# Performance work log

Hardware: AMD Instinct MI355X
Metric: run time of the kernel (lower is better)

## Reference

```python
import jax, jax.numpy as jnp
import numpy as np

IN_DIM = 1024
HEAD_DIM = 64
NUM_HEADS = 16
SEQ = 4096


def setup_inputs() -> dict:
    key = jax.random.key(0)
    ks = jax.random.split(key, 7)
    s = 1.0 / np.sqrt(IN_DIM)
    return {
        "h": jax.random.normal(ks[0], (SEQ, IN_DIM), dtype=jnp.float32),
        "Wq": jax.random.uniform(ks[1], (IN_DIM, NUM_HEADS * HEAD_DIM), jnp.float32, -s, s),
        "Wk": jax.random.uniform(ks[2], (IN_DIM, NUM_HEADS * HEAD_DIM), jnp.float32, -s, s),
        "Wv": jax.random.uniform(ks[3], (IN_DIM, NUM_HEADS * HEAD_DIM), jnp.float32, -s, s),
        "bq": jax.random.uniform(ks[4], (NUM_HEADS * HEAD_DIM,), jnp.float32, -s, s),
        "bk": jax.random.uniform(ks[5], (NUM_HEADS * HEAD_DIM,), jnp.float32, -s, s),
        "bv": jax.random.uniform(ks[6], (NUM_HEADS * HEAD_DIM,), jnp.float32, -s, s),
    }


def reference(h, Wq, Wk, Wv, bq, bk, bv):
    n = h.shape[0]
    # QKV projections -> [H, S, D]
    q = (h @ Wq + bq).reshape(n, NUM_HEADS, HEAD_DIM).transpose(1, 0, 2)
    k = (h @ Wk + bk).reshape(n, NUM_HEADS, HEAD_DIM).transpose(1, 0, 2)
    v = (h @ Wv + bv).reshape(n, NUM_HEADS, HEAD_DIM).transpose(1, 0, 2)
    scale = 1.0 / np.sqrt(HEAD_DIM).astype(np.float32)
    scores = jnp.einsum('hsd,htd->hst', q, k) * scale  # [H, S, S]
    probs = jax.nn.softmax(scores, axis=-1)
    out = jnp.einsum('hst,htd->hsd', probs, v)  # [H, S, D]
    return out.transpose(1, 0, 2).reshape(n, NUM_HEADS * HEAD_DIM)
```

## Files before the change

kernel.cpp:

```cpp
#include <hip/hip_runtime.h>
#include <hip/hip_bf16.h>

#define IN_DIM    1024
#define HEAD_DIM  64
#define NUM_HEADS 16
#define SEQ       4096

#define QSCALE 0.18033688011112042f

typedef __bf16 bf16;
typedef __attribute__((ext_vector_type(4))) __bf16 bf16x4;
typedef __attribute__((ext_vector_type(8))) __bf16 bf16x8;
typedef __attribute__((ext_vector_type(4))) float floatx4;
typedef __attribute__((ext_vector_type(16))) float floatx16;
typedef __attribute__((ext_vector_type(4))) unsigned uint32x4;

__device__ __forceinline__ void async16(bf16* lds, const bf16* g) {
    __builtin_amdgcn_global_load_lds(
        (const __attribute__((address_space(1))) unsigned int*)g,
        (__attribute__((address_space(3))) unsigned int*)lds, 16, 0, 0);
}

__device__ __forceinline__ unsigned cvtpk_bf16(float lo, float hi) {
    unsigned r;
    asm("v_cvt_pk_bf16_f32 %0, %1, %2" : "=v"(r) : "v"(lo), "v"(hi));
    return r;
}

__device__ __forceinline__ void permswap(unsigned& a, unsigned& b) {
    asm("v_permlane32_swap_b32 %0, %1" : "+v"(a), "+v"(b));
}


__global__ void mha_conv_h(const float* __restrict__ h, bf16* __restrict__ hb) {
    int i = blockIdx.x * blockDim.x + threadIdx.x;
    float4 v = ((const float4*)h)[i];
    bf16x4 r;
    r[0] = (bf16)v.x; r[1] = (bf16)v.y; r[2] = (bf16)v.z; r[3] = (bf16)v.w;
    ((bf16x4*)hb)[i] = r;
}

__global__ void mha_conv_wt(const float* __restrict__ Wq, const float* __restrict__ Wk,
                            const float* __restrict__ Wv, bf16* __restrict__ Wt) {
    __shared__ bf16 tile[64][65];
    const int mat = blockIdx.z;
    const float* W = (mat == 0) ? Wq : (mat == 1) ? Wk : Wv;
    const int k0 = blockIdx.y * 64, n0 = blockIdx.x * 64;
    const int tn = threadIdx.x & 63, tq = threadIdx.x >> 6;
#pragma unroll
    for (int i = 0; i < 16; ++i) {
        int kk = tq + i * 4;
        tile[kk][tn] = (bf16)W[(size_t)(k0 + kk) * 1024 + n0 + tn];
    }
    __syncthreads();
#pragma unroll
    for (int i = 0; i < 16; ++i) {
        int nn = tq + i * 4;
        Wt[((size_t)mat << 20) + (size_t)(n0 + nn) * 1024 + k0 + tn] = tile[tn][nn];
    }
}

__launch_bounds__(256)
__global__ void mha_qkv_gemm(const bf16* __restrict__ hb, const bf16* __restrict__ Wt,
                             const float* __restrict__ bq, const float* __restrict__ bk,
                             const float* __restrict__ bv,
                             bf16* __restrict__ Qb, bf16* __restrict__ Kb,
                             bf16* __restrict__ Vt) {
    __shared__ __align__(16) bf16 As[128 * 32];
    __shared__ __align__(16) bf16 Bs[128 * 32];

    const int lane = threadIdx.x & 63;
    const int wave = threadIdx.x >> 6;
    const int l16  = lane & 15;
    const int quad = lane >> 4;
    const int wm   = wave & 1;
    const int wn   = wave >> 1;

    const int m0  = blockIdx.x * 128;
    const int n0  = blockIdx.y * 128;
    const int mat = n0 >> 10;
    const int nc0 = n0 & 1023;

    const bf16* Wp = Wt + ((size_t)mat << 20);

    floatx4 acc[4][4] = {};
    const int swz = (l16 >> 1) & 3;

    for (int k0 = 0; k0 < IN_DIM; k0 += 32) {
#pragma unroll
        for (int r = 0; r < 2; ++r) {
            int g = wave * 128 + r * 64 + lane;
            int row = g >> 2, c = g & 3;
            int gc = c ^ ((row >> 1) & 3);
            bf16* ldsbase_a = As + (size_t)(wave * 128 + r * 64) * 8;
            bf16* ldsbase_b = Bs + (size_t)(wave * 128 + r * 64) * 8;
            async16(ldsbase_a, hb + (size_t)(m0 + row) * IN_DIM + k0 + gc * 8);
            async16(ldsbase_b, Wp + (size_t)(nc0 + row) * IN_DIM + k0 + gc * 8);
        }
        __syncthreads();

        bf16x8 af[4], bf[4];
#pragma unroll
        for (int mt = 0; mt < 4; ++mt)
            af[mt] = *(const bf16x8*)(As + (size_t)(wm * 64 + mt * 16 + l16) * 32
                                      + ((quad ^ swz) * 8));
#pragma unroll
        for (int nt = 0; nt < 4; ++nt)
            bf[nt] = *(const bf16x8*)(Bs + (size_t)(wn * 64 + nt * 16 + l16) * 32
                                      + ((quad ^ swz) * 8));
#pragma unroll
        for (int mt = 0; mt < 4; ++mt)
#pragma unroll
            for (int nt = 0; nt < 4; ++nt)
                acc[mt][nt] = __builtin_amdgcn_mfma_f32_16x16x32_bf16(af[mt], bf[nt],
                                                                      acc[mt][nt], 0, 0, 0);
        __syncthreads();
    }

    const float* bias = (mat == 0) ? bq : (mat == 1) ? bk : bv;
#pragma unroll
    for (int nt = 0; nt < 4; ++nt) {
        int nc = nc0 + wn * 64 + nt * 16 + l16;
        float bb = bias[nc];
        int head = nc >> 6, d = nc & 63;
#pragma unroll
        for (int mt = 0; mt < 4; ++mt)
#pragma unroll
            for (int r = 0; r < 4; ++r) {
                int srow = m0 + wm * 64 + mt * 16 + quad * 4 + r;
                float v = acc[mt][nt][r] + bb;
                if (mat == 0)
                    Qb[((size_t)head * SEQ + srow) * HEAD_DIM + d] = (bf16)(v * QSCALE);
                else if (mat == 1)
                    Kb[((size_t)head * SEQ + srow) * HEAD_DIM + d] = (bf16)v;
                else
                    Vt[((size_t)head * HEAD_DIM + d) * SEQ + srow] = (bf16)v;
            }
    }
}

__launch_bounds__(512)
__global__ void mha_attn(const bf16* __restrict__ Qb, const bf16* __restrict__ Kb,
                         const bf16* __restrict__ Vt, float* __restrict__ out) {
    __shared__ __align__(16) bf16 Ks[3][64 * 64];
    __shared__ __align__(16) bf16 Vs[3][64 * 64];

    const int lane = threadIdx.x & 63;
    const int wave = threadIdx.x >> 6;
    const int l31  = lane & 31;
    const int hi   = lane >> 5;

    const int bid = blockIdx.x;
    const int hh  = 2 * (bid & 7) + ((bid >> 3) & 1);
    const int qx  = bid >> 4;
    const int q0  = qx * 256 + wave * 32;

    const bf16* Qh = Qb + (size_t)hh * SEQ * HEAD_DIM;
    const bf16* Kh = Kb + (size_t)hh * SEQ * HEAD_DIM;
    const bf16* Vh = Vt + (size_t)hh * HEAD_DIM * SEQ;

    const int sg   = wave * 64 + lane;
    const int srow = sg >> 3;
    const int sgc  = (sg & 7) ^ (srow & 7);

    bf16x8 qf[4];
#pragma unroll
    for (int ks = 0; ks < 4; ++ks)
        qf[ks] = *(const bf16x8*)(Qh + (size_t)(q0 + l31) * HEAD_DIM + ks * 16 + hi * 8);

    bf16x8 vone;
#pragma unroll
    for (int i = 0; i < 8; ++i) vone[i] = (bf16)1.0f;

    floatx16 o0 = {}, o1 = {}, ol = {};
    const int swz = l31 & 7;

    async16(&Ks[0][wave * 512], Kh + (size_t)srow * HEAD_DIM + sgc * 8);
    async16(&Vs[0][wave * 512], Vh + (size_t)srow * SEQ + 0 + sgc * 8);
    async16(&Ks[1][wave * 512], Kh + (size_t)(64 + srow) * HEAD_DIM + sgc * 8);
    async16(&Vs[1][wave * 512], Vh + (size_t)srow * SEQ + 64 + sgc * 8);
    asm volatile("s_waitcnt vmcnt(0)" ::: "memory");
    __builtin_amdgcn_s_barrier();

    int cur = 0;
    for (int t = 0; t < SEQ / 64; ++t) {
        int pre = cur + 2; if (pre >= 3) pre -= 3;
        if (t + 2 < SEQ / 64) {
            const int tg = (t + 2) * 64;
            async16(&Ks[pre][wave * 512], Kh + (size_t)(tg + srow) * HEAD_DIM + sgc * 8);
            async16(&Vs[pre][wave * 512], Vh + (size_t)srow * SEQ + tg + sgc * 8);
        }
        if (t < SEQ / 64 - 2)      asm volatile("s_waitcnt vmcnt(4)" ::: "memory");
        else if (t == SEQ / 64 - 2) asm volatile("s_waitcnt vmcnt(2)" ::: "memory");
        else                        asm volatile("s_waitcnt vmcnt(0)" ::: "memory");
        __builtin_amdgcn_s_barrier();
        asm volatile("" ::: "memory");

        bf16x8 kf[2][4];
#pragma unroll
        for (int tt = 0; tt < 2; ++tt)
#pragma unroll
            for (int ks = 0; ks < 4; ++ks)
                kf[tt][ks] = *(const bf16x8*)(&Ks[cur][(tt * 32 + l31) * 64
                                              + (((ks * 2 + hi) ^ swz) * 8)]);

        floatx16 s0 = {}, s1 = {};
#pragma unroll
        for (int ks = 0; ks < 4; ++ks)
            s0 = __builtin_amdgcn_mfma_f32_32x32x16_bf16(kf[0][ks], qf[ks], s0, 0, 0, 0);
#pragma unroll
        for (int ks = 0; ks < 4; ++ks)
            s1 = __builtin_amdgcn_mfma_f32_32x32x16_bf16(kf[1][ks], qf[ks], s1, 0, 0, 0);

        bf16x8 vf[2][4];
#pragma unroll
        for (int dt = 0; dt < 2; ++dt)
#pragma unroll
            for (int sl = 0; sl < 4; ++sl)
                vf[dt][sl] = *(const bf16x8*)(&Vs[cur][(dt * 32 + l31) * 64
                                              + (((sl * 2 + hi) ^ swz) * 8)]);

        bf16x8 pa[4];
#pragma unroll
        for (int sl = 0; sl < 4; ++sl) {
            const floatx16 sv = (sl < 2) ? s0 : s1;
            const int rb = 8 * (sl & 1);
            float p0 = __builtin_amdgcn_exp2f(sv[rb + 0]);
            float p1 = __builtin_amdgcn_exp2f(sv[rb + 1]);
            float p2 = __builtin_amdgcn_exp2f(sv[rb + 2]);
            float p3 = __builtin_amdgcn_exp2f(sv[rb + 3]);
            float p4 = __builtin_amdgcn_exp2f(sv[rb + 4]);
            float p5 = __builtin_amdgcn_exp2f(sv[rb + 5]);
            float p6 = __builtin_amdgcn_exp2f(sv[rb + 6]);
            float p7 = __builtin_amdgcn_exp2f(sv[rb + 7]);
            unsigned u0 = cvtpk_bf16(p0, p1);
            unsigned u1 = cvtpk_bf16(p2, p3);
            unsigned u2 = cvtpk_bf16(p4, p5);
            unsigned u3 = cvtpk_bf16(p6, p7);
            permswap(u0, u2);
            permswap(u1, u3);
            uint32x4 w;
            w[0] = u0; w[1] = u1; w[2] = u2; w[3] = u3;
            pa[sl] = __builtin_bit_cast(bf16x8, w);
        }

#pragma unroll
        for (int sl = 0; sl < 4; ++sl) {
            o0 = __builtin_amdgcn_mfma_f32_32x32x16_bf16(pa[sl], vf[0][sl], o0, 0, 0, 0);
            o1 = __builtin_amdgcn_mfma_f32_32x32x16_bf16(pa[sl], vf[1][sl], o1, 0, 0, 0);
            ol = __builtin_amdgcn_mfma_f32_32x32x16_bf16(pa[sl], vone, ol, 0, 0, 0);
        }

        asm volatile("" ::: "memory");
        __builtin_amdgcn_s_barrier();
        cur = cur + 1; if (cur == 3) cur = 0;
    }

#pragma unroll
    for (int r = 0; r < 16; ++r) {
        const int q = q0 + (r & 3) + 8 * (r >> 2) + 4 * hi;
        const float inv = 1.0f / ol[r];
        out[(size_t)q * (NUM_HEADS * HEAD_DIM) + hh * 64 + l31]      = o0[r] * inv;
        out[(size_t)q * (NUM_HEADS * HEAD_DIM) + hh * 64 + 32 + l31] = o1[r] * inv;
    }
}

extern "C" void kernel_launch(void* const* d_in, const int* in_sizes, int n_in,
                              void* d_out, int out_size, void* d_ws, size_t ws_size,
                              hipStream_t stream) {
    const float* h  = (const float*)d_in[0];
    const float* Wq = (const float*)d_in[1];
    const float* Wk = (const float*)d_in[2];
    const float* Wv = (const float*)d_in[3];
    const float* bq = (const float*)d_in[4];
    const float* bk = (const float*)d_in[5];
    const float* bv = (const float*)d_in[6];
    float* out = (float*)d_out;

    char* ws = (char*)d_ws;
    const size_t MB = 1024 * 1024;
    bf16* hb = (bf16*)(ws);
    bf16* Wt = (bf16*)(ws + 8 * MB);
    bf16* Qb = (bf16*)(ws + 14 * MB);
    bf16* Kb = (bf16*)(ws + 22 * MB);
    bf16* Vt = (bf16*)(ws + 30 * MB);

    mha_conv_h<<<(SEQ * IN_DIM / 4) / 256, 256, 0, stream>>>(h, hb);
    mha_conv_wt<<<dim3(16, 16, 3), 256, 0, stream>>>(Wq, Wk, Wv, Wt);
    mha_qkv_gemm<<<dim3(SEQ / 128, (3 * IN_DIM) / 128), 256, 0, stream>>>(
        hb, Wt, bq, bk, bv, Qb, Kb, Vt);
    mha_attn<<<dim3((SEQ / 256) * NUM_HEADS), 512, 0, stream>>>(Qb, Kb, Vt, out);
}
```

Baseline: 206.5 us.

## Split attention KV range across two blocks and merge with atomics

Each attention block now processes only half of the key/value sequence, doubling the grid to 512 blocks so each CU can host more waves. Partial unnormalized outputs and denominators are combined with float atomicAdd into zeroed workspace buffers, and a separate kernel normalizes into the output. This trades better occupancy and latency hiding for extra zeroing, atomic traffic, and a normalization pass over the full output.

```diff
diff --git a/kernel.cpp b/kernel.cpp
--- a/kernel.cpp
+++ b/kernel.cpp
@@ -31,6 +31,13 @@
     asm("v_permlane32_swap_b32 %0, %1" : "+v"(a), "+v"(b));
 }
 
+
+__global__ void mha_zero(float4* __restrict__ p, int n4) {
+    const float4 z = {0.f, 0.f, 0.f, 0.f};
+    for (int i = blockIdx.x * blockDim.x + threadIdx.x; i < n4;
+         i += gridDim.x * blockDim.x)
+        p[i] = z;
+}
 
 __global__ void mha_conv_h(const float* __restrict__ h, bf16* __restrict__ hb) {
     int i = blockIdx.x * blockDim.x + threadIdx.x;
@@ -139,9 +146,12 @@
     }
 }
 
+#define NT (SEQ / 64 / 2)
+
 __launch_bounds__(512)
 __global__ void mha_attn(const bf16* __restrict__ Qb, const bf16* __restrict__ Kb,
-                         const bf16* __restrict__ Vt, float* __restrict__ out) {
+                         const bf16* __restrict__ Vt, float* __restrict__ num,
+                         float* __restrict__ denom) {
     __shared__ __align__(16) bf16 Ks[3][64 * 64];
     __shared__ __align__(16) bf16 Vs[3][64 * 64];
 
@@ -150,10 +160,14 @@
     const int l31  = lane & 31;
     const int hi   = lane >> 5;
 
-    const int bid = blockIdx.x;
-    const int hh  = 2 * (bid & 7) + ((bid >> 3) & 1);
-    const int qx  = bid >> 4;
-    const int q0  = qx * 256 + wave * 32;
+    const int bid  = blockIdx.x;
+    const int xcd  = bid & 7;
+    const int inner = bid >> 3;
+    const int hh   = 2 * xcd + (inner & 1);
+    const int half = (inner >> 1) & 1;
+    const int qx   = inner >> 2;
+    const int q0   = qx * 256 + wave * 32;
+    const int tb   = half * (SEQ / 2);
 
     const bf16* Qh = Qb + (size_t)hh * SEQ * HEAD_DIM;
     const bf16* Kh = Kb + (size_t)hh * SEQ * HEAD_DIM;
@@ -175,24 +189,24 @@
     floatx16 o0 = {}, o1 = {}, ol = {};
     const int swz = l31 & 7;
 
-    async16(&Ks[0][wave * 512], Kh + (size_t)srow * HEAD_DIM + sgc * 8);
-    async16(&Vs[0][wave * 512], Vh + (size_t)srow * SEQ + 0 + sgc * 8);
-    async16(&Ks[1][wave * 512], Kh + (size_t)(64 + srow) * HEAD_DIM + sgc * 8);
-    async16(&Vs[1][wave * 512], Vh + (size_t)srow * SEQ + 64 + sgc * 8);
+    async16(&Ks[0][wave * 512], Kh + (size_t)(tb + srow) * HEAD_DIM + sgc * 8);
+    async16(&Vs[0][wave * 512], Vh + (size_t)srow * SEQ + tb + sgc * 8);
+    async16(&Ks[1][wave * 512], Kh + (size_t)(tb + 64 + srow) * HEAD_DIM + sgc * 8);
+    async16(&Vs[1][wave * 512], Vh + (size_t)srow * SEQ + tb + 64 + sgc * 8);
     asm volatile("s_waitcnt vmcnt(0)" ::: "memory");
     __builtin_amdgcn_s_barrier();
 
     int cur = 0;
-    for (int t = 0; t < SEQ / 64; ++t) {
+    for (int t = 0; t < NT; ++t) {
         int pre = cur + 2; if (pre >= 3) pre -= 3;
-        if (t + 2 < SEQ / 64) {
-            const int tg = (t + 2) * 64;
+        if (t + 2 < NT) {
+            const int tg = tb + (t + 2) * 64;
             async16(&Ks[pre][wave * 512], Kh + (size_t)(tg + srow) * HEAD_DIM + sgc * 8);
             async16(&Vs[pre][wave * 512], Vh + (size_t)srow * SEQ + tg + sgc * 8);
         }
-        if (t < SEQ / 64 - 2)      asm volatile("s_waitcnt vmcnt(4)" ::: "memory");
-        else if (t == SEQ / 64 - 2) asm volatile("s_waitcnt vmcnt(2)" ::: "memory");
-        else                        asm volatile("s_waitcnt vmcnt(0)" ::: "memory");
+        if (t < NT - 2)       asm volatile("s_waitcnt vmcnt(4)" ::: "memory");
+        else if (t == NT - 2) asm volatile("s_waitcnt vmcnt(2)" ::: "memory");
+        else                  asm volatile("s_waitcnt vmcnt(0)" ::: "memory");
         __builtin_amdgcn_s_barrier();
         asm volatile("" ::: "memory");
 
@@ -259,10 +273,23 @@
 #pragma unroll
     for (int r = 0; r < 16; ++r) {
         const int q = q0 + (r & 3) + 8 * (r >> 2) + 4 * hi;
-        const float inv = 1.0f / ol[r];
-        out[(size_t)q * (NUM_HEADS * HEAD_DIM) + hh * 64 + l31]      = o0[r] * inv;
-        out[(size_t)q * (NUM_HEADS * HEAD_DIM) + hh * 64 + 32 + l31] = o1[r] * inv;
-    }
+        float* np = num + (size_t)q * (NUM_HEADS * HEAD_DIM) + hh * 64;
+        atomicAdd(np + l31,      o0[r]);
+        atomicAdd(np + 32 + l31, o1[r]);
+        if (l31 == 0) atomicAdd(&denom[hh * SEQ + q], ol[r]);
+    }
+}
+
+__global__ void mha_norm(const float* __restrict__ num, const float* __restrict__ denom,
+                         float* __restrict__ out) {
+    const int i = blockIdx.x * blockDim.x + threadIdx.x;
+    const int flat = i * 4;
+    const int q = flat >> 10;
+    const int head = (flat & 1023) >> 6;
+    float4 n = ((const float4*)num)[i];
+    const float inv = 1.0f / denom[head * SEQ + q];
+    n.x *= inv; n.y *= inv; n.z *= inv; n.w *= inv;
+    ((float4*)out)[i] = n;
 }
 
 extern "C" void kernel_launch(void* const* d_in, const int* in_sizes, int n_in,
@@ -279,15 +306,20 @@
 
     char* ws = (char*)d_ws;
     const size_t MB = 1024 * 1024;
-    bf16* hb = (bf16*)(ws);
-    bf16* Wt = (bf16*)(ws + 8 * MB);
-    bf16* Qb = (bf16*)(ws + 14 * MB);
-    bf16* Kb = (bf16*)(ws + 22 * MB);
-    bf16* Vt = (bf16*)(ws + 30 * MB);
-
+    bf16*  hb    = (bf16*)(ws);
+    bf16*  Wt    = (bf16*)(ws + 8 * MB);
+    bf16*  Qb    = (bf16*)(ws + 14 * MB);
+    bf16*  Kb    = (bf16*)(ws + 22 * MB);
+    bf16*  Vt    = (bf16*)(ws + 30 * MB);
+    float* num   = (float*)(ws + 38 * MB);
+    float* denom = (float*)(ws + 54 * MB);
+
+    const int n4 = (16 * 1024 * 1024 + NUM_HEADS * SEQ * 4) / 16;
+    mha_zero<<<2048, 256, 0, stream>>>((float4*)num, n4);
     mha_conv_h<<<(SEQ * IN_DIM / 4) / 256, 256, 0, stream>>>(h, hb);
     mha_conv_wt<<<dim3(16, 16, 3), 256, 0, stream>>>(Wq, Wk, Wv, Wt);
     mha_qkv_gemm<<<dim3(SEQ / 128, (3 * IN_DIM) / 128), 256, 0, stream>>>(
         hb, Wt, bq, bk, bv, Qb, Kb, Vt);
-    mha_attn<<<dim3((SEQ / 256) * NUM_HEADS), 512, 0, stream>>>(Qb, Kb, Vt, out);
-}
+    mha_attn<<<dim3(512), 512, 0, stream>>>(Qb, Kb, Vt, num, denom);
+    mha_norm<<<(SEQ * NUM_HEADS * HEAD_DIM / 4) / 256, 256, 0, stream>>>(num, denom, out);
+}
```

Measured after the change: 226.7 us. 9.8% more time.

## Rewrite QKV GEMM with 256x256 tiles, double-buffered LDS and interleaved prefetch

Applied to the files above, without the earlier changes.

The QKV projection GEMM moves from 128x128 tiles with K-step 32 and two barriers per step to 256x256 tiles with K-step 64 over 512 threads. LDS is double-buffered, and global-to-LDS copies of the next K slice are spread across four MFMA phases, with s_setprio raised around the MFMA bursts. The aim is more data reuse per tile and overlap of memory latency with compute. In exchange the grid shrinks to 192 blocks (fewer than the CU count) and register pressure rises with 32 accumulators per wave.

```diff
diff --git a/kernel.cpp b/kernel.cpp
--- a/kernel.cpp
+++ b/kernel.cpp
@@ -60,74 +60,111 @@
     }
 }
 
-__launch_bounds__(256)
+#define GPHASE(KS, MH, READBF)                                                 \
+    {                                                                          \
+        bf16x8 af[4];                                                          \
+        _Pragma("unroll")                                                      \
+        for (int mtl = 0; mtl < 4; ++mtl)                                      \
+            af[mtl] = *(const bf16x8*)(&Abuf[cb][                              \
+                (wm * 128 + ((MH) * 4 + mtl) * 16 + l16) * 64                  \
+                + ((((KS) * 4 + quad) ^ swz) * 8)]);                           \
+        if (READBF) {                                                          \
+            _Pragma("unroll")                                                  \
+            for (int nt = 0; nt < 4; ++nt)                                     \
+                bfr[nt] = *(const bf16x8*)(&Bbuf[cb][                          \
+                    (wn * 64 + nt * 16 + l16) * 64                             \
+                    + ((((KS) * 4 + quad) ^ swz) * 8)]);                       \
+        }                                                                      \
+        __builtin_amdgcn_s_setprio(1);                                         \
+        _Pragma("unroll")                                                      \
+        for (int mtl = 0; mtl < 4; ++mtl)                                      \
+            _Pragma("unroll")                                                  \
+            for (int nt = 0; nt < 4; ++nt)                                     \
+                acc[(MH) * 4 + mtl][nt] =                                      \
+                    __builtin_amdgcn_mfma_f32_16x16x32_bf16(                   \
+                        af[mtl], bfr[nt], acc[(MH) * 4 + mtl][nt], 0, 0, 0);   \
+        __builtin_amdgcn_s_setprio(0);                                         \
+        asm volatile("" ::: "memory");                                         \
+        __builtin_amdgcn_s_barrier();                                          \
+    }
+
+__launch_bounds__(512)
 __global__ void mha_qkv_gemm(const bf16* __restrict__ hb, const bf16* __restrict__ Wt,
                              const float* __restrict__ bq, const float* __restrict__ bk,
                              const float* __restrict__ bv,
                              bf16* __restrict__ Qb, bf16* __restrict__ Kb,
                              bf16* __restrict__ Vt) {
-    __shared__ __align__(16) bf16 As[128 * 32];
-    __shared__ __align__(16) bf16 Bs[128 * 32];
-
-    const int lane = threadIdx.x & 63;
-    const int wave = threadIdx.x >> 6;
+    __shared__ __align__(16) bf16 Abuf[2][256 * 64];
+    __shared__ __align__(16) bf16 Bbuf[2][256 * 64];
+
+    const int tid  = threadIdx.x;
+    const int lane = tid & 63;
+    const int wave = tid >> 6;
     const int l16  = lane & 15;
-    const int quad = lane >> 4;
-    const int wm   = wave & 1;
-    const int wn   = wave >> 1;
-
-    const int m0  = blockIdx.x * 128;
-    const int n0  = blockIdx.y * 128;
-    const int mat = n0 >> 10;
-    const int nc0 = n0 & 1023;
-
-    const bf16* Wp = Wt + ((size_t)mat << 20);
-
-    floatx4 acc[4][4] = {};
-    const int swz = (l16 >> 1) & 3;
-
-    for (int k0 = 0; k0 < IN_DIM; k0 += 32) {
-#pragma unroll
-        for (int r = 0; r < 2; ++r) {
-            int g = wave * 128 + r * 64 + lane;
-            int row = g >> 2, c = g & 3;
-            int gc = c ^ ((row >> 1) & 3);
-            bf16* ldsbase_a = As + (size_t)(wave * 128 + r * 64) * 8;
-            bf16* ldsbase_b = Bs + (size_t)(wave * 128 + r * 64) * 8;
-            async16(ldsbase_a, hb + (size_t)(m0 + row) * IN_DIM + k0 + gc * 8);
-            async16(ldsbase_b, Wp + (size_t)(nc0 + row) * IN_DIM + k0 + gc * 8);
+    const int quad = (lane >> 4) & 3;
+    const int wm   = wave >> 2;
+    const int wn   = wave & 3;
+
+    const int m0  = blockIdx.x * 256;
+    const int by  = blockIdx.y;
+    const int mat = by >> 2;
+    const int nc0 = (by & 3) * 256;
+
+    const bf16* hb_blk = hb + (size_t)m0 * 1024;
+    const bf16* Wb_blk = Wt + ((size_t)mat << 20) + (size_t)nc0 * 1024;
+
+    const int crow = tid >> 3;
+    const int cs   = (tid & 7) ^ (crow & 7);
+    const int swz  = l16 & 7;
+
+    auto stage_half = [&](bf16* ldsb, const bf16* g) {
+        async16(ldsb + wave * 512,        g + (size_t)crow * 1024 + cs * 8);
+        async16(ldsb + 4096 + wave * 512, g + (size_t)(crow + 64) * 1024 + cs * 8);
+    };
+
+    floatx4 acc[8][4] = {};
+
+    stage_half(&Abuf[0][0],    hb_blk);
+    stage_half(&Abuf[0][8192], hb_blk + 128 * 1024);
+    stage_half(&Bbuf[0][0],    Wb_blk);
+    stage_half(&Bbuf[0][8192], Wb_blk + 128 * 1024);
+
+    for (int u = 0; u < 16; ++u) {
+        const int cb = u & 1, nb = cb ^ 1;
+        const size_t kn = (size_t)(u + 1) * 64;
+        bf16x8 bfr[4];
+
+        if (u < 15) {
+            stage_half(&Abuf[nb][0], hb_blk + kn);
+            asm volatile("s_waitcnt vmcnt(2)" ::: "memory");
+        } else {
+            asm volatile("s_waitcnt vmcnt(0)" ::: "memory");
         }
-        __syncthreads();
-
-        bf16x8 af[4], bf[4];
-#pragma unroll
-        for (int mt = 0; mt < 4; ++mt)
-            af[mt] = *(const bf16x8*)(As + (size_t)(wm * 64 + mt * 16 + l16) * 32
-                                      + ((quad ^ swz) * 8));
-#pragma unroll
-        for (int nt = 0; nt < 4; ++nt)
-            bf[nt] = *(const bf16x8*)(Bs + (size_t)(wn * 64 + nt * 16 + l16) * 32
-                                      + ((quad ^ swz) * 8));
-#pragma unroll
-        for (int mt = 0; mt < 4; ++mt)
-#pragma unroll
-            for (int nt = 0; nt < 4; ++nt)
-                acc[mt][nt] = __builtin_amdgcn_mfma_f32_16x16x32_bf16(af[mt], bf[nt],
-                                                                      acc[mt][nt], 0, 0, 0);
-        __syncthreads();
+        __builtin_amdgcn_s_barrier();
+        asm volatile("" ::: "memory");
+        GPHASE(0, 0, 1)
+
+        if (u < 15) stage_half(&Abuf[nb][8192], hb_blk + 128 * 1024 + kn);
+        GPHASE(0, 1, 0)
+
+        if (u < 15) stage_half(&Bbuf[nb][0], Wb_blk + kn);
+        GPHASE(1, 0, 1)
+
+        if (u < 15) stage_half(&Bbuf[nb][8192], Wb_blk + 128 * 1024 + kn);
+        GPHASE(1, 1, 0)
     }
 
     const float* bias = (mat == 0) ? bq : (mat == 1) ? bk : bv;
+    const int head = (nc0 >> 6) + wn;
 #pragma unroll
     for (int nt = 0; nt < 4; ++nt) {
-        int nc = nc0 + wn * 64 + nt * 16 + l16;
-        float bb = bias[nc];
-        int head = nc >> 6, d = nc & 63;
-#pragma unroll
-        for (int mt = 0; mt < 4; ++mt)
+        const int d  = nt * 16 + l16;
+        const float bb = bias[nc0 + wn * 64 + d];
+#pragma unroll
+        for (int mt = 0; mt < 8; ++mt)
 #pragma unroll
             for (int r = 0; r < 4; ++r) {
-                int srow = m0 + wm * 64 + mt * 16 + quad * 4 + r;
+                const int srow = m0 + wm * 128 + mt * 16 + quad * 4 + r;
                 float v = acc[mt][nt][r] + bb;
                 if (mat == 0)
                     Qb[((size_t)head * SEQ + srow) * HEAD_DIM + d] = (bf16)(v * QSCALE);
@@ -190,7 +227,7 @@
             async16(&Ks[pre][wave * 512], Kh + (size_t)(tg + srow) * HEAD_DIM + sgc * 8);
             async16(&Vs[pre][wave * 512], Vh + (size_t)srow * SEQ + tg + sgc * 8);
         }
-        if (t < SEQ / 64 - 2)      asm volatile("s_waitcnt vmcnt(4)" ::: "memory");
+        if (t < SEQ / 64 - 2)       asm volatile("s_waitcnt vmcnt(4)" ::: "memory");
         else if (t == SEQ / 64 - 2) asm volatile("s_waitcnt vmcnt(2)" ::: "memory");
         else                        asm volatile("s_waitcnt vmcnt(0)" ::: "memory");
         __builtin_amdgcn_s_barrier();
@@ -287,7 +324,7 @@
 
     mha_conv_h<<<(SEQ * IN_DIM / 4) / 256, 256, 0, stream>>>(h, hb);
     mha_conv_wt<<<dim3(16, 16, 3), 256, 0, stream>>>(Wq, Wk, Wv, Wt);
-    mha_qkv_gemm<<<dim3(SEQ / 128, (3 * IN_DIM) / 128), 256, 0, stream>>>(
+    mha_qkv_gemm<<<dim3(16, 12), 512, 0, stream>>>(
         hb, Wt, bq, bk, bv, Qb, Kb, Vt);
     mha_attn<<<dim3((SEQ / 256) * NUM_HEADS), 512, 0, stream>>>(Qb, Kb, Vt, out);
 }
```

Result: slower. 242.2 us (+17.3%).

## Give each attention wave 64 query rows, halving waves per block

Applied to the files above, without the earlier changes.

The attention kernel now runs 4 waves of 256 threads instead of 8, and each wave processes two 32-row query tiles that share the same K/V fragments read from LDS. This halves LDS reads of K and V per query row and doubles the cooperative load work per thread. It also makes the cvt and permlane inline asm volatile with explicit s_nop padding, which pins instruction ordering. In exchange it raises register pressure (launch bounds 256,1) and leaves fewer waves per CU to hide latency.

```diff
diff --git a/kernel.cpp b/kernel.cpp
--- a/kernel.cpp
+++ b/kernel.cpp
@@ -23,13 +23,38 @@
 
 __device__ __forceinline__ unsigned cvtpk_bf16(float lo, float hi) {
     unsigned r;
-    asm("v_cvt_pk_bf16_f32 %0, %1, %2" : "=v"(r) : "v"(lo), "v"(hi));
+    asm volatile("s_nop 1\n\tv_cvt_pk_bf16_f32 %0, %1, %2"
+                 : "=v"(r) : "v"(lo), "v"(hi));
     return r;
 }
 
 __device__ __forceinline__ void permswap(unsigned& a, unsigned& b) {
-    asm("v_permlane32_swap_b32 %0, %1" : "+v"(a), "+v"(b));
-}
+    asm volatile("s_nop 3\n\tv_permlane32_swap_b32 %0, %1" : "+v"(a), "+v"(b));
+}
+
+#define PACK(PA, S0, S1)                                                       \
+    _Pragma("unroll")                                                          \
+    for (int sl = 0; sl < 4; ++sl) {                                           \
+        const floatx16 sv = (sl < 2) ? (S0) : (S1);                            \
+        const int rb = 8 * (sl & 1);                                           \
+        float p0 = __builtin_amdgcn_exp2f(sv[rb + 0]);                         \
+        float p1 = __builtin_amdgcn_exp2f(sv[rb + 1]);                         \
+        float p2 = __builtin_amdgcn_exp2f(sv[rb + 2]);                         \
+        float p3 = __builtin_amdgcn_exp2f(sv[rb + 3]);                         \
+        float p4 = __builtin_amdgcn_exp2f(sv[rb + 4]);                         \
+        float p5 = __builtin_amdgcn_exp2f(sv[rb + 5]);                         \
+        float p6 = __builtin_amdgcn_exp2f(sv[rb + 6]);                         \
+        float p7 = __builtin_amdgcn_exp2f(sv[rb + 7]);                         \
+        unsigned u0 = cvtpk_bf16(p0, p1);                                      \
+        unsigned u1 = cvtpk_bf16(p2, p3);                                      \
+        unsigned u2 = cvtpk_bf16(p4, p5);                                      \
+        unsigned u3 = cvtpk_bf16(p6, p7);                                      \
+        permswap(u0, u2);                                                      \
+        permswap(u1, u3);                                                      \
+        uint32x4 w;                                                            \
+        w[0] = u0; w[1] = u1; w[2] = u2; w[3] = u3;                            \
+        (PA)[sl] = __builtin_bit_cast(bf16x8, w);                              \
+    }
 
 
 __global__ void mha_conv_h(const float* __restrict__ h, bf16* __restrict__ hb) {
@@ -139,7 +164,7 @@
     }
 }
 
-__launch_bounds__(512)
+__launch_bounds__(256, 1)
 __global__ void mha_attn(const bf16* __restrict__ Qb, const bf16* __restrict__ Kb,
                          const bf16* __restrict__ Vt, float* __restrict__ out) {
     __shared__ __align__(16) bf16 Ks[3][64 * 64];
@@ -153,32 +178,44 @@
     const int bid = blockIdx.x;
     const int hh  = 2 * (bid & 7) + ((bid >> 3) & 1);
     const int qx  = bid >> 4;
-    const int q0  = qx * 256 + wave * 32;
+    const int q0  = qx * 256 + wave * 64;
 
     const bf16* Qh = Qb + (size_t)hh * SEQ * HEAD_DIM;
     const bf16* Kh = Kb + (size_t)hh * SEQ * HEAD_DIM;
     const bf16* Vh = Vt + (size_t)hh * HEAD_DIM * SEQ;
 
-    const int sg   = wave * 64 + lane;
-    const int srow = sg >> 3;
-    const int sgc  = (sg & 7) ^ (srow & 7);
-
-    bf16x8 qf[4];
-#pragma unroll
-    for (int ks = 0; ks < 4; ++ks)
-        qf[ks] = *(const bf16x8*)(Qh + (size_t)(q0 + l31) * HEAD_DIM + ks * 16 + hi * 8);
+    const int ci0 = wave * 64 + lane;
+    const int r0c = ci0 >> 3;
+    const int sc0 = (ci0 & 7) ^ (r0c & 7);
+    const int r1c = r0c + 32;
+    const int sc1 = sc0;
+
+    bf16x8 qfa[4], qfb[4];
+#pragma unroll
+    for (int ks = 0; ks < 4; ++ks) {
+        qfa[ks] = *(const bf16x8*)(Qh + (size_t)(q0 + l31) * HEAD_DIM + ks * 16 + hi * 8);
+        qfb[ks] = *(const bf16x8*)(Qh + (size_t)(q0 + 32 + l31) * HEAD_DIM + ks * 16 + hi * 8);
+    }
 
     bf16x8 vone;
 #pragma unroll
     for (int i = 0; i < 8; ++i) vone[i] = (bf16)1.0f;
 
-    floatx16 o0 = {}, o1 = {}, ol = {};
+    floatx16 o0a = {}, o1a = {}, ola = {};
+    floatx16 o0b = {}, o1b = {}, olb = {};
     const int swz = l31 & 7;
 
-    async16(&Ks[0][wave * 512], Kh + (size_t)srow * HEAD_DIM + sgc * 8);
-    async16(&Vs[0][wave * 512], Vh + (size_t)srow * SEQ + 0 + sgc * 8);
-    async16(&Ks[1][wave * 512], Kh + (size_t)(64 + srow) * HEAD_DIM + sgc * 8);
-    async16(&Vs[1][wave * 512], Vh + (size_t)srow * SEQ + 64 + sgc * 8);
+    auto stageK = [&](int buf, int t0) {
+        async16(&Ks[buf][wave * 512],        Kh + (size_t)(t0 + r0c) * HEAD_DIM + sc0 * 8);
+        async16(&Ks[buf][2048 + wave * 512], Kh + (size_t)(t0 + r1c) * HEAD_DIM + sc1 * 8);
+    };
+    auto stageV = [&](int buf, int t0) {
+        async16(&Vs[buf][wave * 512],        Vh + (size_t)r0c * SEQ + t0 + sc0 * 8);
+        async16(&Vs[buf][2048 + wave * 512], Vh + (size_t)r1c * SEQ + t0 + sc1 * 8);
+    };
+
+    stageK(0, 0);  stageV(0, 0);
+    stageK(1, 64); stageV(1, 64);
     asm volatile("s_waitcnt vmcnt(0)" ::: "memory");
     __builtin_amdgcn_s_barrier();
 
@@ -186,12 +223,11 @@
     for (int t = 0; t < SEQ / 64; ++t) {
         int pre = cur + 2; if (pre >= 3) pre -= 3;
         if (t + 2 < SEQ / 64) {
-            const int tg = (t + 2) * 64;
-            async16(&Ks[pre][wave * 512], Kh + (size_t)(tg + srow) * HEAD_DIM + sgc * 8);
-            async16(&Vs[pre][wave * 512], Vh + (size_t)srow * SEQ + tg + sgc * 8);
-        }
-        if (t < SEQ / 64 - 2)      asm volatile("s_waitcnt vmcnt(4)" ::: "memory");
-        else if (t == SEQ / 64 - 2) asm volatile("s_waitcnt vmcnt(2)" ::: "memory");
+            stageK(pre, (t + 2) * 64);
+            stageV(pre, (t + 2) * 64);
+        }
+        if (t < SEQ / 64 - 2)       asm volatile("s_waitcnt vmcnt(8)" ::: "memory");
+        else if (t == SEQ / 64 - 2) asm volatile("s_waitcnt vmcnt(4)" ::: "memory");
         else                        asm volatile("s_waitcnt vmcnt(0)" ::: "memory");
         __builtin_amdgcn_s_barrier();
         asm volatile("" ::: "memory");
@@ -204,14 +240,6 @@
                 kf[tt][ks] = *(const bf16x8*)(&Ks[cur][(tt * 32 + l31) * 64
                                               + (((ks * 2 + hi) ^ swz) * 8)]);
 
-        floatx16 s0 = {}, s1 = {};
-#pragma unroll
-        for (int ks = 0; ks < 4; ++ks)
-            s0 = __builtin_amdgcn_mfma_f32_32x32x16_bf16(kf[0][ks], qf[ks], s0, 0, 0, 0);
-#pragma unroll
-        for (int ks = 0; ks < 4; ++ks)
-            s1 = __builtin_amdgcn_mfma_f32_32x32x16_bf16(kf[1][ks], qf[ks], s1, 0, 0, 0);
-
         bf16x8 vf[2][4];
 #pragma unroll
         for (int dt = 0; dt < 2; ++dt)
@@ -220,35 +248,34 @@
                 vf[dt][sl] = *(const bf16x8*)(&Vs[cur][(dt * 32 + l31) * 64
                                               + (((sl * 2 + hi) ^ swz) * 8)]);
 
-        bf16x8 pa[4];
+        floatx16 s0a = {}, s1a = {};
+#pragma unroll
+        for (int ks = 0; ks < 4; ++ks) {
+            s0a = __builtin_amdgcn_mfma_f32_32x32x16_bf16(kf[0][ks], qfa[ks], s0a, 0, 0, 0);
+            s1a = __builtin_amdgcn_mfma_f32_32x32x16_bf16(kf[1][ks], qfa[ks], s1a, 0, 0, 0);
+        }
+        bf16x8 paa[4];
+        PACK(paa, s0a, s1a)
 #pragma unroll
         for (int sl = 0; sl < 4; ++sl) {
-            const floatx16 sv = (sl < 2) ? s0 : s1;
-            const int rb = 8 * (sl & 1);
-            float p0 = __builtin_amdgcn_exp2f(sv[rb + 0]);
-            float p1 = __builtin_amdgcn_exp2f(sv[rb + 1]);
-            float p2 = __builtin_amdgcn_exp2f(sv[rb + 2]);
-            float p3 = __builtin_amdgcn_exp2f(sv[rb + 3]);
-            float p4 = __builtin_amdgcn_exp2f(sv[rb + 4]);
-            float p5 = __builtin_amdgcn_exp2f(sv[rb + 5]);
-            float p6 = __builtin_amdgcn_exp2f(sv[rb + 6]);
-            float p7 = __builtin_amdgcn_exp2f(sv[rb + 7]);
-            unsigned u0 = cvtpk_bf16(p0, p1);
-            unsigned u1 = cvtpk_bf16(p2, p3);
-            unsigned u2 = cvtpk_bf16(p4, p5);
-            unsigned u3 = cvtpk_bf16(p6, p7);
-            permswap(u0, u2);
-            permswap(u1, u3);
-            uint32x4 w;
-            w[0] = u0; w[1] = u1; w[2] = u2; w[3] = u3;
-            pa[sl] = __builtin_bit_cast(bf16x8, w);
-        }
-
+            o0a = __builtin_amdgcn_mfma_f32_32x32x16_bf16(paa[sl], vf[0][sl], o0a, 0, 0, 0);
+            o1a = __builtin_amdgcn_mfma_f32_32x32x16_bf16(paa[sl], vf[1][sl], o1a, 0, 0, 0);
+            ola = __builtin_amdgcn_mfma_f32_32x32x16_bf16(paa[sl], vone,      ola, 0, 0, 0);
+        }
+
+        floatx16 s0b = {}, s1b = {};
+#pragma unroll
+        for (int ks = 0; ks < 4; ++ks) {
+            s0b = __builtin_amdgcn_mfma_f32_32x32x16_bf16(kf[0][ks], qfb[ks], s0b, 0, 0, 0);
+            s1b = __builtin_amdgcn_mfma_f32_32x32x16_bf16(kf[1][ks], qfb[ks], s1b, 0, 0, 0);
+        }
+        bf16x8 pab[4];
+        PACK(pab, s0b, s1b)
 #pragma unroll
         for (int sl = 0; sl < 4; ++sl) {
-            o0 = __builtin_amdgcn_mfma_f32_32x32x16_bf16(pa[sl], vf[0][sl], o0, 0, 0, 0);
-            o1 = __builtin_amdgcn_mfma_f32_32x32x16_bf16(pa[sl], vf[1][sl], o1, 0, 0, 0);
-            ol = __builtin_amdgcn_mfma_f32_32x32x16_bf16(pa[sl], vone, ol, 0, 0, 0);
+            o0b = __builtin_amdgcn_mfma_f32_32x32x16_bf16(pab[sl], vf[0][sl], o0b, 0, 0, 0);
+            o1b = __builtin_amdgcn_mfma_f32_32x32x16_bf16(pab[sl], vf[1][sl], o1b, 0, 0, 0);
+            olb = __builtin_amdgcn_mfma_f32_32x32x16_bf16(pab[sl], vone,      olb, 0, 0, 0);
         }
 
         asm volatile("" ::: "memory");
@@ -258,10 +285,14 @@
 
 #pragma unroll
     for (int r = 0; r < 16; ++r) {
-        const int q = q0 + (r & 3) + 8 * (r >> 2) + 4 * hi;
-        const float inv = 1.0f / ol[r];
-        out[(size_t)q * (NUM_HEADS * HEAD_DIM) + hh * 64 + l31]      = o0[r] * inv;
-        out[(size_t)q * (NUM_HEADS * HEAD_DIM) + hh * 64 + 32 + l31] = o1[r] * inv;
+        const int qa = q0 + (r & 3) + 8 * (r >> 2) + 4 * hi;
+        const float inva = 1.0f / ola[r];
+        out[(size_t)qa * (NUM_HEADS * HEAD_DIM) + hh * 64 + l31]      = o0a[r] * inva;
+        out[(size_t)qa * (NUM_HEADS * HEAD_DIM) + hh * 64 + 32 + l31] = o1a[r] * inva;
+        const int qb = qa + 32;
+        const float invb = 1.0f / olb[r];
+        out[(size_t)qb * (NUM_HEADS * HEAD_DIM) + hh * 64 + l31]      = o0b[r] * invb;
+        out[(size_t)qb * (NUM_HEADS * HEAD_DIM) + hh * 64 + 32 + l31] = o1b[r] * invb;
     }
 }
 
@@ -289,5 +320,5 @@
     mha_conv_wt<<<dim3(16, 16, 3), 256, 0, stream>>>(Wq, Wk, Wv, Wt);
     mha_qkv_gemm<<<dim3(SEQ / 128, (3 * IN_DIM) / 128), 256, 0, stream>>>(
         hb, Wt, bq, bk, bv, Qb, Kb, Vt);
-    mha_attn<<<dim3((SEQ / 256) * NUM_HEADS), 512, 0, stream>>>(Qb, Kb, Vt, out);
-}
+    mha_attn<<<dim3((SEQ / 256) * NUM_HEADS), 256, 0, stream>>>(Qb, Kb, Vt, out);
+}
```

After: 257.6 us. +24.7%, slower.
